# Kernel tuning notes

Hardware: AMD Instinct MI355X
Metric: run time of the kernel (lower is better)

Reference implementation:

```python
import jax, jax.numpy as jnp
import numpy as np

K, T, F = 30000, 48, 4
EPS = 1e-5  # torch BatchNorm1d default eps


def _bn_params(key, c):
    k1, k2, k3, k4 = jax.random.split(key, 4)
    g = jax.random.uniform(k1, (c,), jnp.float32, 0.5, 1.5)
    b = jax.random.normal(k2, (c,), jnp.float32) * 0.1
    m = jax.random.normal(k3, (c,), jnp.float32) * 0.1
    v = jax.random.uniform(k4, (c,), jnp.float32, 0.5, 1.5)
    return g, b, m, v


def setup_inputs() -> dict:
    key = jax.random.key(0)
    ks = jax.random.split(key, 12)
    features = jax.random.normal(ks[0], (K, T, F), jnp.float32)
    # at least 1 valid point per non-empty voxel
    num_voxels = jnp.maximum(jax.random.randint(ks[1], (K,), 0, T), 1).astype(jnp.int32)
    coors = jax.random.randint(ks[2], (K, 3), 0, 100).astype(jnp.int32)
    # VFE1: in=8 (4 + 3 rel + 1 dist), units = 32//2 = 16
    w1 = jax.random.normal(ks[3], (8, 16), jnp.float32) / np.sqrt(8)
    b1 = jax.random.normal(ks[4], (16,), jnp.float32) * 0.01
    g1, be1, m1, v1 = _bn_params(ks[5], 16)
    # VFE2: in=32, units = 128//2 = 64
    w2 = jax.random.normal(ks[6], (32, 64), jnp.float32) / np.sqrt(32)
    b2 = jax.random.normal(ks[7], (64,), jnp.float32) * 0.01
    g2, be2, m2, v2 = _bn_params(ks[8], 64)
    # final linear 128 -> 128
    w3 = jax.random.normal(ks[9], (128, 128), jnp.float32) / np.sqrt(128)
    b3 = jax.random.normal(ks[10], (128,), jnp.float32) * 0.01
    g3, be3, m3, v3 = _bn_params(ks[11], 128)
    return dict(features=features, num_voxels=num_voxels, coors=coors,
                w1=w1, b1=b1, g1=g1, be1=be1, m1=m1, v1=v1,
                w2=w2, b2=b2, g2=g2, be2=be2, m2=m2, v2=v2,
                w3=w3, b3=b3, g3=g3, be3=be3, m3=m3, v3=v3)


def _bn(x, g, b, m, v):
    # eval-mode BatchNorm over last (channel) axis
    return (x - m) * (g / jnp.sqrt(v + EPS)) + b


def _vfe(x, W, b, g, be, m, v):
    # x: [K, T, Cin] -> [K, T, 2*units]
    h = jax.nn.relu(_bn(jnp.einsum('ktc,cu->ktu', x, W) + b, g, be, m, v))
    agg = jnp.max(h, axis=1, keepdims=True)  # [K, 1, U]
    return jnp.concatenate([h, jnp.broadcast_to(agg, h.shape)], axis=2)


def reference(features, num_voxels, coors,
              w1, b1, g1, be1, m1, v1,
              w2, b2, g2, be2, m2, v2,
              w3, b3, g3, be3, m3, v3):
    xyz = features[:, :, :3]
    nv = num_voxels.astype(features.dtype)[:, None, None]
    points_mean = jnp.sum(xyz, axis=1, keepdims=True) / nv
    rel = xyz - points_mean
    dist = jnp.linalg.norm(xyz, axis=2, keepdims=True)
    x = jnp.concatenate([features, rel, dist], axis=-1)  # [K, T, 8]
    mask = (jnp.arange(T)[None, :] < num_voxels[:, None]).astype(features.dtype)[:, :, None]
    x = x * mask
    x = _vfe(x, w1, b1, g1, be1, m1, v1) * mask   # [K, T, 32]
    x = _vfe(x, w2, b2, g2, be2, m2, v2) * mask   # [K, T, 128]
    x = jax.nn.relu(_bn(jnp.einsum('ktc,cu->ktu', x, w3) + b3, g3, be3, m3, v3)) * mask
    return jnp.max(x, axis=1)  # [K, 128]
```

## Files before the change

kernel.cpp:

```cpp
#include <hip/hip_runtime.h>

constexpr float EPS = 1e-5f;

typedef __attribute__((ext_vector_type(8))) short bf16x8;
typedef __attribute__((ext_vector_type(4))) float f32x4;

#define W2P_OFF 32768
#define W1P_OFF 40960
#define B1_OFF  41984
#define B2_OFF  42048
#define B3_OFF  42304

#define APAD 20

__device__ __forceinline__ ushort f2bf(float x) {
    union { float f; unsigned u; } a; a.f = x;
    unsigned r = a.u + 0x7fffu + ((a.u >> 16) & 1u);
    return (ushort)(r >> 16);
}

__device__ __forceinline__ unsigned cvtpk(float lo, float hi) {
    unsigned r;
    asm("v_cvt_pk_bf16_f32 %0, %1, %2" : "=v"(r) : "v"(lo), "v"(hi));
    return r;
}

__global__ void vfe_prep(
    const float* __restrict__ w1, const float* __restrict__ b1,
    const float* __restrict__ g1, const float* __restrict__ be1,
    const float* __restrict__ m1, const float* __restrict__ v1,
    const float* __restrict__ w2, const float* __restrict__ b2,
    const float* __restrict__ g2, const float* __restrict__ be2,
    const float* __restrict__ m2, const float* __restrict__ v2,
    const float* __restrict__ w3, const float* __restrict__ b3,
    const float* __restrict__ g3, const float* __restrict__ be3,
    const float* __restrict__ m3, const float* __restrict__ v3,
    void* __restrict__ ws)
{
    ushort* w3p = (ushort*)ws;
    ushort* w2p = (ushort*)((char*)ws + W2P_OFF);
    ushort* w1p = (ushort*)((char*)ws + W1P_OFF);
    float*  bb1 = (float*)((char*)ws + B1_OFF);
    float*  bb2 = (float*)((char*)ws + B2_OFF);
    float*  bb3 = (float*)((char*)ws + B3_OFF);

    const int i = blockIdx.x * 256 + threadIdx.x;
    if (i < 16384) {
        const int e = i & 7, l = (i >> 3) & 63, rest = i >> 9;
        const int ks = rest & 3, nt = rest >> 2, g = l >> 4;
        const int k = ks * 32 + g * 8 + e;
        const int n = nt * 16 + (l & 15);
        const float s = g3[n] * rsqrtf(v3[n] + EPS);
        w3p[i] = f2bf(w3[k * 128 + n] * s);
    } else if (i < 20480) {
        const int j = i - 16384;
        const int e = j & 7, l = (j >> 3) & 63, rest = j >> 9;
        const int nt = rest & 3, sel = rest >> 2;
        const int klog = (l >> 4) * 8 + e;
        const int n = nt * 16 + (l & 15);
        const float s = g2[n] * rsqrtf(v2[n] + EPS);
        w2p[j] = (klog < 16) ? f2bf(w2[(sel * 16 + klog) * 64 + n] * s) : (ushort)0;
    } else if (i < 20992) {
        const int j = i - 20480;
        const int e = j & 7, l = j >> 3;
        const int klog = (l >> 4) * 8 + e;
        const int u = l & 15;
        const float s = g1[u] * rsqrtf(v1[u] + EPS);
        w1p[j] = (klog < 8) ? f2bf(w1[klog * 16 + u] * s) : (ushort)0;
    } else if (i < 21200) {
        const int j = i - 20992;
        if (j < 16) {
            const int u = j;
            bb1[u] = (b1[u] - m1[u]) * (g1[u] * rsqrtf(v1[u] + EPS)) + be1[u];
        } else if (j < 80) {
            const int u = j - 16;
            bb2[u] = (b2[u] - m2[u]) * (g2[u] * rsqrtf(v2[u] + EPS)) + be2[u];
        } else {
            const int u = j - 80;
            bb3[u] = (b3[u] - m3[u]) * (g3[u] * rsqrtf(v3[u] + EPS)) + be3[u];
        }
    }
}

#define NV(v)   ((v)==0?nv0:(v)==1?nv1:(v)==2?nv2:nv3)
#define LIM(v)  ((v)==0?lim0:(v)==1?lim1:(v)==2?lim2:lim3)
#define FULL(v) ((v)==0?full0:(v)==1?full1:(v)==2?full2:full3)

__global__ __launch_bounds__(256, 4) void vfe_fused(
    const float* __restrict__ feat,
    const int* __restrict__ nvox,
    const void* __restrict__ ws,
    float* __restrict__ out,
    int K)
{
    __shared__ __align__(16) ushort sBfrag[12 * 2 * 64 * 8];
    __shared__ __align__(16) ushort sAfrag[12 * 16 * APAD];
    __shared__ __align__(16) ushort sAgg1bf[4][16];
    __shared__ __align__(16) ushort sAgg2bf[4][64];

    ushort (*sX0bf)[8] = (ushort(*)[8])&sBfrag[0];

    const ushort* w3p = (const ushort*)ws;
    const ushort* w2p = (const ushort*)((const char*)ws + W2P_OFF);
    const ushort* w1p = (const ushort*)((const char*)ws + W1P_OFF);
    const float*  bb1 = (const float*)((const char*)ws + B1_OFF);
    const float*  bb2 = (const float*)((const char*)ws + B2_OFF);
    const float*  bb3 = (const float*)((const char*)ws + B3_OFF);

    const int tid  = threadIdx.x;
    const int lane = tid & 63;
    const int w    = tid >> 6;
    const int g    = lane >> 4;
    const int m15  = lane & 15;
    const int kA   = blockIdx.x * 4;

    int kk0 = kA, kk1 = min(kA+1, K-1), kk2 = min(kA+2, K-1), kk3 = min(kA+3, K-1);
    int nv0 = __builtin_amdgcn_readfirstlane(nvox[kk0]);
    int nv1 = __builtin_amdgcn_readfirstlane(nvox[kk1]);
    int nv2 = __builtin_amdgcn_readfirstlane(nvox[kk2]);
    int nv3 = __builtin_amdgcn_readfirstlane(nvox[kk3]);
    const int lim0=(nv0+15)>>4, lim1=(nv1+15)>>4, lim2=(nv2+15)>>4, lim3=(nv3+15)>>4;
    const int full0=nv0>>4, full1=nv1>>4, full2=nv2>>4, full3=nv3>>4;

    union U8 { bf16x8 v; unsigned u[4]; };

    const bf16x8 b1f   = *(const bf16x8*)(w1p + (size_t)lane * 8);
    const bf16x8 w2lof = *(const bf16x8*)(w2p + (size_t)((0 * 4 + w) * 64 + lane) * 8);
    const bf16x8 w2hif = *(const bf16x8*)(w2p + (size_t)((1 * 4 + w) * 64 + lane) * 8);
    bf16x8 b3f[2][4];
    #pragma unroll
    for (int nt = 0; nt < 2; ++nt)
        #pragma unroll
        for (int ks = 0; ks < 4; ++ks)
            b3f[nt][ks] = *(const bf16x8*)(w3p + (size_t)(((w * 2 + nt) * 4 + ks) * 64 + lane) * 8);

    {
        const int kkw = (w==0)?kk0:(w==1)?kk1:(w==2)?kk2:kk3;
        const int nvw = (w==0)?nv0:(w==1)?nv1:(w==2)?nv2:nv3;
        float4 f = make_float4(0.f, 0.f, 0.f, 0.f);
        if (lane < 48)
            f = *reinterpret_cast<const float4*>(feat + ((size_t)kkw * 48 + lane) * 4);
        float sx = f.x, sy = f.y, sz = f.z;
        #pragma unroll
        for (int d = 1; d < 64; d <<= 1) {
            sx += __shfl_xor(sx, d);
            sy += __shfl_xor(sy, d);
            sz += __shfl_xor(sz, d);
        }
        const float inv = 1.f / (float)nvw;
        if (lane < 48) {
            const float msk = (lane < nvw) ? 1.f : 0.f;
            const float dd = sqrtf(f.x * f.x + f.y * f.y + f.z * f.z);
            U8 a;
            a.u[0] = cvtpk(f.x * msk, f.y * msk);
            a.u[1] = cvtpk(f.z * msk, f.w * msk);
            a.u[2] = cvtpk((f.x - sx * inv) * msk, (f.y - sy * inv) * msk);
            a.u[3] = cvtpk((f.z - sz * inv) * msk, dd * msk);
            *reinterpret_cast<bf16x8*>(&sX0bf[w * 48 + lane][0]) = a.v;
        }
    }

    {
        const float bb1u = bb1[m15];
        const int limw = (w==0)?lim0:(w==1)?lim1:(w==2)?lim2:lim3;
        const f32x4 ci = {bb1u, bb1u, bb1u, bb1u};
        float pmax = fmaxf(bb1u, 0.f);
        #pragma unroll
        for (int s = 0; s < 3; ++s) {
            if (s < limw) {
                const bf16x8 af = *(const bf16x8*)&sX0bf[w * 48 + s * 16 + m15][0];
                f32x4 acc = __builtin_amdgcn_mfma_f32_16x16x32_bf16(af, b1f, ci, 0, 0, 0);
                float h0 = fmaxf(acc[0], 0.f), h1 = fmaxf(acc[1], 0.f);
                float h2 = fmaxf(acc[2], 0.f), h3 = fmaxf(acc[3], 0.f);
                pmax = fmaxf(pmax, fmaxf(fmaxf(h0, h1), fmaxf(h2, h3)));
                const unsigned p01 = cvtpk(h0, h1), p23 = cvtpk(h2, h3);
                ushort* base = &sAfrag[((w * 3 + s) * 16 + g * 4) * APAD + m15];
                base[0 * APAD] = (ushort)p01;
                base[1 * APAD] = (ushort)(p01 >> 16);
                base[2 * APAD] = (ushort)p23;
                base[3 * APAD] = (ushort)(p23 >> 16);
            }
        }
        pmax = fmaxf(pmax, __shfl_xor(pmax, 16));
        pmax = fmaxf(pmax, __shfl_xor(pmax, 32));
        if (g == 0) sAgg1bf[w][m15] = f2bf(pmax);
    }
    __syncthreads();

    const int col2 = w * 16 + m15;
    const float bb2c = bb2[col2];
    f32x4 z2acc;
    {
        const bf16x8 az2 = *(const bf16x8*)&sAgg1bf[m15 & 3][(g & 1) * 8];
        f32x4 ci = {bb2c, bb2c, bb2c, bb2c};
        z2acc = __builtin_amdgcn_mfma_f32_16x16x32_bf16(az2, w2hif, ci, 0, 0, 0);
    }

    {
        const int ks = col2 >> 5, gp = (col2 >> 3) & 3, e = col2 & 7;
        #pragma unroll
        for (int vg = 0; vg < 2; ++vg) {
            const f32x4 cP = {z2acc[vg*2],   z2acc[vg*2],   z2acc[vg*2],   z2acc[vg*2]};
            const f32x4 cQ = {z2acc[vg*2+1], z2acc[vg*2+1], z2acc[vg*2+1], z2acc[vg*2+1]};
            f32x4 acc2[6];
            #pragma unroll
            for (int j = 0; j < 6; ++j) {
                const int tt = vg * 6 + j;
                const int vox = vg * 2 + j / 3;
                const int mtl = j % 3;
                if (mtl < LIM(vox)) {
                    const bf16x8 af = *(const bf16x8*)&sAfrag[(tt * 16 + m15) * APAD + (g & 1) * 8];
                    acc2[j] = __builtin_amdgcn_mfma_f32_16x16x32_bf16(af, w2lof, (j < 3) ? cP : cQ, 0, 0, 0);
                }
            }
            float mxP = fmaxf(bb2c, 0.f);
            float mxQ = fmaxf(bb2c, 0.f);
            #pragma unroll
            for (int j = 0; j < 6; ++j) {
                const int tt = vg * 6 + j;
                const int vox = vg * 2 + j / 3;
                const int mtl = j % 3;
                if (mtl < LIM(vox)) {
                    float h[4];
                    #pragma unroll
                    for (int r = 0; r < 4; ++r) h[r] = fmaxf(acc2[j][r], 0.f);
                    const unsigned p01 = cvtpk(h[0], h[1]), p23 = cvtpk(h[2], h[3]);
                    ushort* base = &sBfrag[((tt * 2 + ks) * 64 + gp * 16 + g * 4) * 8 + e];
                    base[0]  = (ushort)p01;
                    base[8]  = (ushort)(p01 >> 16);
                    base[16] = (ushort)p23;
                    base[24] = (ushort)(p23 >> 16);
                    if (mtl < FULL(vox)) {
                        const float t01 = fmaxf(h[0], h[1]), t23 = fmaxf(h[2], h[3]);
                        if (j < 3) mxP = fmaxf(mxP, fmaxf(t01, t23));
                        else       mxQ = fmaxf(mxQ, fmaxf(t01, t23));
                    } else {
                        #pragma unroll
                        for (int r = 0; r < 4; ++r) {
                            if (mtl * 16 + g * 4 + r < NV(vox)) {
                                if (j < 3) mxP = fmaxf(mxP, h[r]);
                                else       mxQ = fmaxf(mxQ, h[r]);
                            }
                        }
                    }
                }
            }
            mxP = fmaxf(mxP, __shfl_xor(mxP, 16));
            mxP = fmaxf(mxP, __shfl_xor(mxP, 32));
            mxQ = fmaxf(mxQ, __shfl_xor(mxQ, 16));
            mxQ = fmaxf(mxQ, __shfl_xor(mxQ, 32));
            if (g == 0) {
                sAgg2bf[vg * 2 + 0][col2] = f2bf(mxP);
                sAgg2bf[vg * 2 + 1][col2] = f2bf(mxQ);
            }
        }
    }
    __syncthreads();

    f32x4 i3[2];
    #pragma unroll
    for (int nt = 0; nt < 2; ++nt) {
        const float bb3c = bb3[(w * 2 + nt) * 16 + m15];
        f32x4 z = {bb3c, bb3c, bb3c, bb3c};
        #pragma unroll
        for (int ks2 = 0; ks2 < 2; ++ks2) {
            const bf16x8 af = *(const bf16x8*)&sAgg2bf[m15 & 3][ks2 * 32 + g * 8];
            z = __builtin_amdgcn_mfma_f32_16x16x32_bf16(af, b3f[nt][2 + ks2], z, 0, 0, 0);
        }
        i3[nt] = z;
    }

    #pragma unroll
    for (int pass = 0; pass < 2; ++pass) {
        const int col = (w * 2 + pass) * 16 + m15;
        #pragma unroll
        for (int vg = 0; vg < 2; ++vg) {
            const f32x4 cP = {i3[pass][vg*2],   i3[pass][vg*2],   i3[pass][vg*2],   i3[pass][vg*2]};
            const f32x4 cQ = {i3[pass][vg*2+1], i3[pass][vg*2+1], i3[pass][vg*2+1], i3[pass][vg*2+1]};
            f32x4 acc3[6];
            __builtin_amdgcn_s_setprio(1);
            #pragma unroll
            for (int j = 0; j < 6; ++j) {
                const int tt = vg * 6 + j;
                const int vox = vg * 2 + j / 3;
                const int mtl = j % 3;
                if (mtl < LIM(vox)) {
                    const bf16x8 af0 = *(const bf16x8*)&sBfrag[((tt * 2 + 0) * 64 + lane) * 8];
                    const bf16x8 af1 = *(const bf16x8*)&sBfrag[((tt * 2 + 1) * 64 + lane) * 8];
                    acc3[j] = __builtin_amdgcn_mfma_f32_16x16x32_bf16(af0, b3f[pass][0], (j < 3) ? cP : cQ, 0, 0, 0);
                    acc3[j] = __builtin_amdgcn_mfma_f32_16x16x32_bf16(af1, b3f[pass][1], acc3[j], 0, 0, 0);
                }
            }
            __builtin_amdgcn_s_setprio(0);
            float mxP = 0.f, mxQ = 0.f;
            #pragma unroll
            for (int j = 0; j < 6; ++j) {
                const int vox = vg * 2 + j / 3;
                const int mtl = j % 3;
                if (mtl < FULL(vox)) {
                    const float t01 = fmaxf(acc3[j][0], acc3[j][1]);
                    const float t23 = fmaxf(acc3[j][2], acc3[j][3]);
                    if (j < 3) mxP = fmaxf(mxP, fmaxf(t01, t23));
                    else       mxQ = fmaxf(mxQ, fmaxf(t01, t23));
                } else if (mtl < LIM(vox)) {
                    #pragma unroll
                    for (int r = 0; r < 4; ++r) {
                        if (mtl * 16 + g * 4 + r < NV(vox)) {
                            if (j < 3) mxP = fmaxf(mxP, acc3[j][r]);
                            else       mxQ = fmaxf(mxQ, acc3[j][r]);
                        }
                    }
                }
            }
            mxP = fmaxf(mxP, __shfl_xor(mxP, 16));
            mxP = fmaxf(mxP, __shfl_xor(mxP, 32));
            mxQ = fmaxf(mxQ, __shfl_xor(mxQ, 16));
            mxQ = fmaxf(mxQ, __shfl_xor(mxQ, 32));
            if (g == (vg * 2 + 0) && (kA + vg * 2 + 0) < K) out[(size_t)(kA + vg * 2 + 0) * 128 + col] = mxP;
            if (g == (vg * 2 + 1) && (kA + vg * 2 + 1) < K) out[(size_t)(kA + vg * 2 + 1) * 128 + col] = mxQ;
        }
    }
}

extern "C" void kernel_launch(void* const* d_in, const int* in_sizes, int n_in,
                              void* d_out, int out_size, void* d_ws, size_t ws_size,
                              hipStream_t stream) {
    const float* feat = (const float*)d_in[0];
    const int*   nvx  = (const int*)d_in[1];
    const float* w1 = (const float*)d_in[3];
    const float* b1 = (const float*)d_in[4];
    const float* g1 = (const float*)d_in[5];
    const float* be1= (const float*)d_in[6];
    const float* m1 = (const float*)d_in[7];
    const float* v1 = (const float*)d_in[8];
    const float* w2 = (const float*)d_in[9];
    const float* b2 = (const float*)d_in[10];
    const float* g2 = (const float*)d_in[11];
    const float* be2= (const float*)d_in[12];
    const float* m2 = (const float*)d_in[13];
    const float* v2 = (const float*)d_in[14];
    const float* w3 = (const float*)d_in[15];
    const float* b3 = (const float*)d_in[16];
    const float* g3 = (const float*)d_in[17];
    const float* be3= (const float*)d_in[18];
    const float* m3 = (const float*)d_in[19];
    const float* v3 = (const float*)d_in[20];
    float* out = (float*)d_out;

    const int K = in_sizes[1];

    vfe_prep<<<84, 256, 0, stream>>>(w1,b1,g1,be1,m1,v1, w2,b2,g2,be2,m2,v2,
                                     w3,b3,g3,be3,m3,v3, d_ws);
    vfe_fused<<<(K + 3) / 4, 256, 0, stream>>>(feat, nvx, d_ws, out, K);
}
```

Baseline: 72.15 us.

## Assign one voxel per wavefront and remove block-level barriers

The kernel now gives each wavefront a single voxel and has it compute every output column for that voxel, instead of splitting columns across wavefronts and sharing four voxels through LDS. Shared buffers are indexed per wave, so both __syncthreads calls are removed. Weight fragments for layers 2 and 3 are loaded from global memory inside the column loops rather than held in registers up front. This drops block-wide synchronisation and the per-voxel select chains, but each wave now reads all weight tiles (more global/L2 traffic) and may use more registers.

New measurement: 86.02 us. 19.2% more time.

```diff
diff --git a/kernel.cpp b/kernel.cpp
--- a/kernel.cpp
+++ b/kernel.cpp
@@ -82,10 +82,6 @@
     }
 }
 
-#define NV(v)   ((v)==0?nv0:(v)==1?nv1:(v)==2?nv2:nv3)
-#define LIM(v)  ((v)==0?lim0:(v)==1?lim1:(v)==2?lim2:lim3)
-#define FULL(v) ((v)==0?full0:(v)==1?full1:(v)==2?full2:full3)
-
 __global__ __launch_bounds__(256, 4) void vfe_fused(
     const float* __restrict__ feat,
     const int* __restrict__ nvox,
@@ -93,12 +89,11 @@
     float* __restrict__ out,
     int K)
 {
-    __shared__ __align__(16) ushort sBfrag[12 * 2 * 64 * 8];
-    __shared__ __align__(16) ushort sAfrag[12 * 16 * APAD];
+    __shared__ __align__(16) ushort sBfrag[4][3 * 2 * 64 * 8];
+    __shared__ __align__(16) ushort sAfrag[4][3 * 16 * APAD];
+    __shared__ __align__(16) ushort sX0bf[4][48 * 8];
     __shared__ __align__(16) ushort sAgg1bf[4][16];
     __shared__ __align__(16) ushort sAgg2bf[4][64];
-
-    ushort (*sX0bf)[8] = (ushort(*)[8])&sBfrag[0];
 
     const ushort* w3p = (const ushort*)ws;
     const ushort* w2p = (const ushort*)((const char*)ws + W2P_OFF);
@@ -112,34 +107,20 @@
     const int w    = tid >> 6;
     const int g    = lane >> 4;
     const int m15  = lane & 15;
-    const int kA   = blockIdx.x * 4;
-
-    int kk0 = kA, kk1 = min(kA+1, K-1), kk2 = min(kA+2, K-1), kk3 = min(kA+3, K-1);
-    int nv0 = __builtin_amdgcn_readfirstlane(nvox[kk0]);
-    int nv1 = __builtin_amdgcn_readfirstlane(nvox[kk1]);
-    int nv2 = __builtin_amdgcn_readfirstlane(nvox[kk2]);
-    int nv3 = __builtin_amdgcn_readfirstlane(nvox[kk3]);
-    const int lim0=(nv0+15)>>4, lim1=(nv1+15)>>4, lim2=(nv2+15)>>4, lim3=(nv3+15)>>4;
-    const int full0=nv0>>4, full1=nv1>>4, full2=nv2>>4, full3=nv3>>4;
+
+    const int kraw = blockIdx.x * 4 + w;
+    const int kc   = min(kraw, K - 1);
+    int nv = nvox[kc];
+    nv = __builtin_amdgcn_readfirstlane(nv);
+    const int lim  = (nv + 15) >> 4;
+    const int full = nv >> 4;
 
     union U8 { bf16x8 v; unsigned u[4]; };
 
-    const bf16x8 b1f   = *(const bf16x8*)(w1p + (size_t)lane * 8);
-    const bf16x8 w2lof = *(const bf16x8*)(w2p + (size_t)((0 * 4 + w) * 64 + lane) * 8);
-    const bf16x8 w2hif = *(const bf16x8*)(w2p + (size_t)((1 * 4 + w) * 64 + lane) * 8);
-    bf16x8 b3f[2][4];
-    #pragma unroll
-    for (int nt = 0; nt < 2; ++nt)
-        #pragma unroll
-        for (int ks = 0; ks < 4; ++ks)
-            b3f[nt][ks] = *(const bf16x8*)(w3p + (size_t)(((w * 2 + nt) * 4 + ks) * 64 + lane) * 8);
-
     {
-        const int kkw = (w==0)?kk0:(w==1)?kk1:(w==2)?kk2:kk3;
-        const int nvw = (w==0)?nv0:(w==1)?nv1:(w==2)?nv2:nv3;
         float4 f = make_float4(0.f, 0.f, 0.f, 0.f);
         if (lane < 48)
-            f = *reinterpret_cast<const float4*>(feat + ((size_t)kkw * 48 + lane) * 4);
+            f = *reinterpret_cast<const float4*>(feat + ((size_t)kc * 48 + lane) * 4);
         float sx = f.x, sy = f.y, sz = f.z;
         #pragma unroll
         for (int d = 1; d < 64; d <<= 1) {
@@ -147,34 +128,34 @@
             sy += __shfl_xor(sy, d);
             sz += __shfl_xor(sz, d);
         }
-        const float inv = 1.f / (float)nvw;
+        const float inv = 1.f / (float)nv;
         if (lane < 48) {
-            const float msk = (lane < nvw) ? 1.f : 0.f;
+            const float msk = (lane < nv) ? 1.f : 0.f;
             const float dd = sqrtf(f.x * f.x + f.y * f.y + f.z * f.z);
             U8 a;
             a.u[0] = cvtpk(f.x * msk, f.y * msk);
             a.u[1] = cvtpk(f.z * msk, f.w * msk);
             a.u[2] = cvtpk((f.x - sx * inv) * msk, (f.y - sy * inv) * msk);
             a.u[3] = cvtpk((f.z - sz * inv) * msk, dd * msk);
-            *reinterpret_cast<bf16x8*>(&sX0bf[w * 48 + lane][0]) = a.v;
+            *reinterpret_cast<bf16x8*>(&sX0bf[w][lane * 8]) = a.v;
         }
     }
 
     {
+        const bf16x8 b1f = *(const bf16x8*)(w1p + (size_t)lane * 8);
         const float bb1u = bb1[m15];
-        const int limw = (w==0)?lim0:(w==1)?lim1:(w==2)?lim2:lim3;
         const f32x4 ci = {bb1u, bb1u, bb1u, bb1u};
         float pmax = fmaxf(bb1u, 0.f);
         #pragma unroll
         for (int s = 0; s < 3; ++s) {
-            if (s < limw) {
-                const bf16x8 af = *(const bf16x8*)&sX0bf[w * 48 + s * 16 + m15][0];
+            if (s < lim) {
+                const bf16x8 af = *(const bf16x8*)&sX0bf[w][(s * 16 + m15) * 8];
                 f32x4 acc = __builtin_amdgcn_mfma_f32_16x16x32_bf16(af, b1f, ci, 0, 0, 0);
                 float h0 = fmaxf(acc[0], 0.f), h1 = fmaxf(acc[1], 0.f);
                 float h2 = fmaxf(acc[2], 0.f), h3 = fmaxf(acc[3], 0.f);
                 pmax = fmaxf(pmax, fmaxf(fmaxf(h0, h1), fmaxf(h2, h3)));
                 const unsigned p01 = cvtpk(h0, h1), p23 = cvtpk(h2, h3);
-                ushort* base = &sAfrag[((w * 3 + s) * 16 + g * 4) * APAD + m15];
+                ushort* base = &sAfrag[w][(s * 16 + g * 4) * APAD + m15];
                 base[0 * APAD] = (ushort)p01;
                 base[1 * APAD] = (ushort)(p01 >> 16);
                 base[2 * APAD] = (ushort)p23;
@@ -185,140 +166,113 @@
         pmax = fmaxf(pmax, __shfl_xor(pmax, 32));
         if (g == 0) sAgg1bf[w][m15] = f2bf(pmax);
     }
-    __syncthreads();
-
-    const int col2 = w * 16 + m15;
-    const float bb2c = bb2[col2];
-    f32x4 z2acc;
+
+    f32x4 z2acc[4];
+    float bb2v[4];
     {
-        const bf16x8 az2 = *(const bf16x8*)&sAgg1bf[m15 & 3][(g & 1) * 8];
-        f32x4 ci = {bb2c, bb2c, bb2c, bb2c};
-        z2acc = __builtin_amdgcn_mfma_f32_16x16x32_bf16(az2, w2hif, ci, 0, 0, 0);
-    }
-
-    {
-        const int ks = col2 >> 5, gp = (col2 >> 3) & 3, e = col2 & 7;
-        #pragma unroll
-        for (int vg = 0; vg < 2; ++vg) {
-            const f32x4 cP = {z2acc[vg*2],   z2acc[vg*2],   z2acc[vg*2],   z2acc[vg*2]};
-            const f32x4 cQ = {z2acc[vg*2+1], z2acc[vg*2+1], z2acc[vg*2+1], z2acc[vg*2+1]};
-            f32x4 acc2[6];
+        const bf16x8 az2 = *(const bf16x8*)&sAgg1bf[w][(g & 1) * 8];
+        #pragma unroll
+        for (int nt = 0; nt < 4; ++nt) {
+            bb2v[nt] = bb2[nt * 16 + m15];
+            const bf16x8 w2hi = *(const bf16x8*)(w2p + (size_t)((4 + nt) * 64 + lane) * 8);
+            f32x4 ci = {bb2v[nt], bb2v[nt], bb2v[nt], bb2v[nt]};
+            z2acc[nt] = __builtin_amdgcn_mfma_f32_16x16x32_bf16(az2, w2hi, ci, 0, 0, 0);
+        }
+    }
+
+    #pragma unroll
+    for (int vh = 0; vh < 2; ++vh) {
+        bf16x8 wlo[2];
+        #pragma unroll
+        for (int j = 0; j < 2; ++j)
+            wlo[j] = *(const bf16x8*)(w2p + (size_t)((vh * 2 + j) * 64 + lane) * 8);
+        f32x4 acc2[3][2];
+        #pragma unroll
+        for (int s = 0; s < 3; ++s) {
+            if (s < lim) {
+                const bf16x8 af = *(const bf16x8*)&sAfrag[w][(s * 16 + m15) * APAD + (g & 1) * 8];
+                #pragma unroll
+                for (int j = 0; j < 2; ++j)
+                    acc2[s][j] = __builtin_amdgcn_mfma_f32_16x16x32_bf16(af, wlo[j], z2acc[vh * 2 + j], 0, 0, 0);
+            }
+        }
+        #pragma unroll
+        for (int j = 0; j < 2; ++j) {
+            const int nt = vh * 2 + j;
+            const int col = nt * 16 + m15;
+            const int ks = col >> 5, gp = (col >> 3) & 3, e = col & 7;
+            float mx = fmaxf(bb2v[nt], 0.f);
             #pragma unroll
-            for (int j = 0; j < 6; ++j) {
-                const int tt = vg * 6 + j;
-                const int vox = vg * 2 + j / 3;
-                const int mtl = j % 3;
-                if (mtl < LIM(vox)) {
-                    const bf16x8 af = *(const bf16x8*)&sAfrag[(tt * 16 + m15) * APAD + (g & 1) * 8];
-                    acc2[j] = __builtin_amdgcn_mfma_f32_16x16x32_bf16(af, w2lof, (j < 3) ? cP : cQ, 0, 0, 0);
-                }
-            }
-            float mxP = fmaxf(bb2c, 0.f);
-            float mxQ = fmaxf(bb2c, 0.f);
-            #pragma unroll
-            for (int j = 0; j < 6; ++j) {
-                const int tt = vg * 6 + j;
-                const int vox = vg * 2 + j / 3;
-                const int mtl = j % 3;
-                if (mtl < LIM(vox)) {
+            for (int s = 0; s < 3; ++s) {
+                if (s < lim) {
                     float h[4];
                     #pragma unroll
-                    for (int r = 0; r < 4; ++r) h[r] = fmaxf(acc2[j][r], 0.f);
+                    for (int r = 0; r < 4; ++r) h[r] = fmaxf(acc2[s][j][r], 0.f);
                     const unsigned p01 = cvtpk(h[0], h[1]), p23 = cvtpk(h[2], h[3]);
-                    ushort* base = &sBfrag[((tt * 2 + ks) * 64 + gp * 16 + g * 4) * 8 + e];
+                    ushort* base = &sBfrag[w][((s * 2 + ks) * 64 + gp * 16 + g * 4) * 8 + e];
                     base[0]  = (ushort)p01;
                     base[8]  = (ushort)(p01 >> 16);
                     base[16] = (ushort)p23;
                     base[24] = (ushort)(p23 >> 16);
-                    if (mtl < FULL(vox)) {
-                        const float t01 = fmaxf(h[0], h[1]), t23 = fmaxf(h[2], h[3]);
-                        if (j < 3) mxP = fmaxf(mxP, fmaxf(t01, t23));
-                        else       mxQ = fmaxf(mxQ, fmaxf(t01, t23));
+                    if (s < full) {
+                        mx = fmaxf(mx, fmaxf(fmaxf(h[0], h[1]), fmaxf(h[2], h[3])));
                     } else {
                         #pragma unroll
-                        for (int r = 0; r < 4; ++r) {
-                            if (mtl * 16 + g * 4 + r < NV(vox)) {
-                                if (j < 3) mxP = fmaxf(mxP, h[r]);
-                                else       mxQ = fmaxf(mxQ, h[r]);
-                            }
-                        }
+                        for (int r = 0; r < 4; ++r)
+                            if (s * 16 + g * 4 + r < nv) mx = fmaxf(mx, h[r]);
                     }
                 }
             }
-            mxP = fmaxf(mxP, __shfl_xor(mxP, 16));
-            mxP = fmaxf(mxP, __shfl_xor(mxP, 32));
-            mxQ = fmaxf(mxQ, __shfl_xor(mxQ, 16));
-            mxQ = fmaxf(mxQ, __shfl_xor(mxQ, 32));
-            if (g == 0) {
-                sAgg2bf[vg * 2 + 0][col2] = f2bf(mxP);
-                sAgg2bf[vg * 2 + 1][col2] = f2bf(mxQ);
-            }
-        }
-    }
-    __syncthreads();
-
-    f32x4 i3[2];
+            mx = fmaxf(mx, __shfl_xor(mx, 16));
+            mx = fmaxf(mx, __shfl_xor(mx, 32));
+            if (g == 0) sAgg2bf[w][col] = f2bf(mx);
+        }
+    }
+
+    bf16x8 a3[3][2];
     #pragma unroll
-    for (int nt = 0; nt < 2; ++nt) {
-        const float bb3c = bb3[(w * 2 + nt) * 16 + m15];
+    for (int s = 0; s < 3; ++s) {
+        if (s < lim) {
+            a3[s][0] = *(const bf16x8*)&sBfrag[w][((s * 2 + 0) * 64 + lane) * 8];
+            a3[s][1] = *(const bf16x8*)&sBfrag[w][((s * 2 + 1) * 64 + lane) * 8];
+        }
+    }
+    const bf16x8 afz0 = *(const bf16x8*)&sAgg2bf[w][0 * 32 + g * 8];
+    const bf16x8 afz1 = *(const bf16x8*)&sAgg2bf[w][1 * 32 + g * 8];
+
+    #pragma unroll 2
+    for (int nt = 0; nt < 8; ++nt) {
+        const int col = nt * 16 + m15;
+        const float bb3c = bb3[col];
+        const bf16x8 b3l0 = *(const bf16x8*)(w3p + (size_t)((nt * 4 + 0) * 64 + lane) * 8);
+        const bf16x8 b3l1 = *(const bf16x8*)(w3p + (size_t)((nt * 4 + 1) * 64 + lane) * 8);
+        const bf16x8 b3h0 = *(const bf16x8*)(w3p + (size_t)((nt * 4 + 2) * 64 + lane) * 8);
+        const bf16x8 b3h1 = *(const bf16x8*)(w3p + (size_t)((nt * 4 + 3) * 64 + lane) * 8);
         f32x4 z = {bb3c, bb3c, bb3c, bb3c};
-        #pragma unroll
-        for (int ks2 = 0; ks2 < 2; ++ks2) {
-            const bf16x8 af = *(const bf16x8*)&sAgg2bf[m15 & 3][ks2 * 32 + g * 8];
-            z = __builtin_amdgcn_mfma_f32_16x16x32_bf16(af, b3f[nt][2 + ks2], z, 0, 0, 0);
-        }
-        i3[nt] = z;
-    }
-
-    #pragma unroll
-    for (int pass = 0; pass < 2; ++pass) {
-        const int col = (w * 2 + pass) * 16 + m15;
-        #pragma unroll
-        for (int vg = 0; vg < 2; ++vg) {
-            const f32x4 cP = {i3[pass][vg*2],   i3[pass][vg*2],   i3[pass][vg*2],   i3[pass][vg*2]};
-            const f32x4 cQ = {i3[pass][vg*2+1], i3[pass][vg*2+1], i3[pass][vg*2+1], i3[pass][vg*2+1]};
-            f32x4 acc3[6];
-            __builtin_amdgcn_s_setprio(1);
-            #pragma unroll
-            for (int j = 0; j < 6; ++j) {
-                const int tt = vg * 6 + j;
-                const int vox = vg * 2 + j / 3;
-                const int mtl = j % 3;
-                if (mtl < LIM(vox)) {
-                    const bf16x8 af0 = *(const bf16x8*)&sBfrag[((tt * 2 + 0) * 64 + lane) * 8];
-                    const bf16x8 af1 = *(const bf16x8*)&sBfrag[((tt * 2 + 1) * 64 + lane) * 8];
-                    acc3[j] = __builtin_amdgcn_mfma_f32_16x16x32_bf16(af0, b3f[pass][0], (j < 3) ? cP : cQ, 0, 0, 0);
-                    acc3[j] = __builtin_amdgcn_mfma_f32_16x16x32_bf16(af1, b3f[pass][1], acc3[j], 0, 0, 0);
-                }
-            }
-            __builtin_amdgcn_s_setprio(0);
-            float mxP = 0.f, mxQ = 0.f;
-            #pragma unroll
-            for (int j = 0; j < 6; ++j) {
-                const int vox = vg * 2 + j / 3;
-                const int mtl = j % 3;
-                if (mtl < FULL(vox)) {
-                    const float t01 = fmaxf(acc3[j][0], acc3[j][1]);
-                    const float t23 = fmaxf(acc3[j][2], acc3[j][3]);
-                    if (j < 3) mxP = fmaxf(mxP, fmaxf(t01, t23));
-                    else       mxQ = fmaxf(mxQ, fmaxf(t01, t23));
-                } else if (mtl < LIM(vox)) {
-                    #pragma unroll
-                    for (int r = 0; r < 4; ++r) {
-                        if (mtl * 16 + g * 4 + r < NV(vox)) {
-                            if (j < 3) mxP = fmaxf(mxP, acc3[j][r]);
-                            else       mxQ = fmaxf(mxQ, acc3[j][r]);
-                        }
-                    }
-                }
-            }
-            mxP = fmaxf(mxP, __shfl_xor(mxP, 16));
-            mxP = fmaxf(mxP, __shfl_xor(mxP, 32));
-            mxQ = fmaxf(mxQ, __shfl_xor(mxQ, 16));
-            mxQ = fmaxf(mxQ, __shfl_xor(mxQ, 32));
-            if (g == (vg * 2 + 0) && (kA + vg * 2 + 0) < K) out[(size_t)(kA + vg * 2 + 0) * 128 + col] = mxP;
-            if (g == (vg * 2 + 1) && (kA + vg * 2 + 1) < K) out[(size_t)(kA + vg * 2 + 1) * 128 + col] = mxQ;
-        }
+        z = __builtin_amdgcn_mfma_f32_16x16x32_bf16(afz0, b3h0, z, 0, 0, 0);
+        z = __builtin_amdgcn_mfma_f32_16x16x32_bf16(afz1, b3h1, z, 0, 0, 0);
+        f32x4 acc3[3];
+        #pragma unroll
+        for (int s = 0; s < 3; ++s) {
+            if (s < lim) {
+                acc3[s] = __builtin_amdgcn_mfma_f32_16x16x32_bf16(a3[s][0], b3l0, z, 0, 0, 0);
+                acc3[s] = __builtin_amdgcn_mfma_f32_16x16x32_bf16(a3[s][1], b3l1, acc3[s], 0, 0, 0);
+            }
+        }
+        float mx = 0.f;
+        #pragma unroll
+        for (int s = 0; s < 3; ++s) {
+            if (s < full) {
+                mx = fmaxf(mx, fmaxf(fmaxf(acc3[s][0], acc3[s][1]), fmaxf(acc3[s][2], acc3[s][3])));
+            } else if (s < lim) {
+                #pragma unroll
+                for (int r = 0; r < 4; ++r)
+                    if (s * 16 + g * 4 + r < nv) mx = fmaxf(mx, acc3[s][r]);
+            }
+        }
+        mx = fmaxf(mx, __shfl_xor(mx, 16));
+        mx = fmaxf(mx, __shfl_xor(mx, 32));
+        if (g == 0 && kraw < K) out[(size_t)kc * 128 + col] = mx;
     }
 }
 
```
